# Performance work log

Hardware: AMD Instinct MI355X
Metric: run time of the kernel (lower is better)

The kernel has to match this reference:

```python
import jax, jax.numpy as jnp
import numpy as np

B, F0, D = 2048, 40, 32
LAYER0, LAYER1 = 128, 128  # layer_size=(128,128), split_half=True -> field_nums=[40,64]


def setup_inputs() -> dict:
    key = jax.random.key(0)
    k1, k2, k3 = jax.random.split(key, 3)
    x = jax.random.normal(k1, (B, F0, D), dtype=jnp.float32)
    # TF conv1d filters: [1, F_prev*F0, size]; we store them reshaped [F0, F_prev_fields, size]
    # Layer 0: F_prev = F0 = 40 -> W0 flattened index m = i*F0 + j, i over x0 fields, j over hidden fields
    W0 = jax.random.normal(k2, (F0, F0, LAYER0), dtype=jnp.float32) * 0.05
    b0 = jnp.zeros((LAYER0,), dtype=jnp.float32)
    # Layer 1: F_prev = LAYER0 // 2 = 64 (split_half)
    W1 = jax.random.normal(k3, (F0, LAYER0 // 2, LAYER1), dtype=jnp.float32) * 0.05
    b1 = jnp.zeros((LAYER1,), dtype=jnp.float32)
    return {"x": x, "W0": W0, "b0": b0, "W1": W1, "b1": b1}


def reference(x, W0, b0, W1, b1):
    # CIN layer 0: outer product x0 (x) x0 over fields per embedding dim, then 1x1 conv + bias + relu
    # TF flattens dot_result as index i*F_prev + j, matching W0[i, j, s].
    h0 = jax.nn.relu(jnp.einsum('bid,bjd,ijs->bsd', x, x, W0) + b0[None, :, None])  # (B, 128, D)
    half = LAYER0 // 2
    next_hidden, direct0 = h0[:, :half, :], h0[:, half:, :]  # split_half
    # CIN layer 1 (last layer): all feature maps go to direct connect
    direct1 = jax.nn.relu(
        jnp.einsum('bid,bjd,ijs->bsd', x, next_hidden, W1) + b1[None, :, None]
    )  # (B, 128, D)
    result = jnp.concatenate([direct0, direct1], axis=1)  # (B, 192, D)
    return jnp.sum(result, axis=-1)  # (B, 192)
```

## Files before the change

kernel.cpp:

```cpp
#include <hip/hip_runtime.h>
#include <stdint.h>


typedef __attribute__((ext_vector_type(8))) _Float16 half8;
typedef __attribute__((ext_vector_type(2))) _Float16 half2v;
typedef __attribute__((ext_vector_type(16))) float f32x16;

#define T0 30
#define T1P 81
#define PERIOD 3
#define WBUF 12288

__host__ __device__ constexpr int ic0_of(int t) {
    return (t < 2) ? t : (t < 6) ? (t - 2) : (t < 12) ? (t - 6)
         : (t < 20) ? (t - 12) : (t - 20);
}
__host__ __device__ constexpr int jc0_of(int t) {
    return (t < 2) ? 0 : (t < 6) ? 1 : (t < 12) ? 2 : (t < 20) ? 3 : 4;
}

__device__ __forceinline__ unsigned short f2h(float f) {
    return __builtin_bit_cast(unsigned short, (_Float16)f);
}
__device__ __forceinline__ void gl_lds16(const unsigned short* g, unsigned short* l) {
    __builtin_amdgcn_global_load_lds(
        (const __attribute__((address_space(1))) unsigned int*)g,
        (__attribute__((address_space(3))) unsigned int*)l,
        16, 0, 0);
}
__device__ __forceinline__ uint4 avmul(half2v xs, uint4 jv) {
    uint4 r;
    r.x = __builtin_bit_cast(unsigned int, (half2v)(xs * __builtin_bit_cast(half2v, jv.x)));
    r.y = __builtin_bit_cast(unsigned int, (half2v)(xs * __builtin_bit_cast(half2v, jv.y)));
    r.z = __builtin_bit_cast(unsigned int, (half2v)(xs * __builtin_bit_cast(half2v, jv.z)));
    r.w = __builtin_bit_cast(unsigned int, (half2v)(xs * __builtin_bit_cast(half2v, jv.w)));
    return r;
}

__global__ void permute_w_both(const float* __restrict__ W0, const float* __restrict__ W1,
                               unsigned short* __restrict__ Wp0, unsigned short* __restrict__ Wp1)
{
    const int t = blockIdx.x;
    const int tid = threadIdx.x;
    unsigned short outv[16];
    unsigned short* dst;
    if (t < T0) {
        const int ic = ic0_of(t), jc = jc0_of(t);
        #pragma unroll
        for (int q = 0; q < 16; ++q) {
            int pos  = tid * 16 + q;
            int e    = pos & 7, lane = (pos >> 3) & 63;
            int kh   = (pos >> 9) & 1, sq = pos >> 10;
            int s    = sq * 32 + (lane & 31);
            int i    = ic * 4 + kh * 2 + (lane >> 5);
            int j    = jc * 8 + e;
            float v = 0.0f;
            if (i < j)       v = W0[((size_t)(i * 40 + j)) * 128 + s]
                               + W0[((size_t)(j * 40 + i)) * 128 + s];
            else if (i == j) v = W0[((size_t)(i * 40 + i)) * 128 + s];
            outv[q] = f2h(v);
        }
        dst = Wp0 + (size_t)t * 4096 + tid * 16;
    } else {
        const int tt = t - T0;
        if (tt == 80) {
            #pragma unroll
            for (int q = 0; q < 16; ++q) outv[q] = 0;
        } else {
            const int jc = tt / 10, ic = tt % 10;
            #pragma unroll
            for (int q = 0; q < 16; ++q) {
                int pos  = tid * 16 + q;
                int e    = pos & 7, lane = (pos >> 3) & 63;
                int kh   = (pos >> 9) & 1, sq = pos >> 10;
                int s    = sq * 32 + (lane & 31);
                int i    = ic * 4 + kh * 2 + (lane >> 5);
                int j    = jc * 8 + e;
                outv[q] = f2h(W1[((size_t)(i * 64 + j)) * 128 + s]);
            }
        }
        dst = Wp1 + (size_t)tt * 4096 + tid * 16;
    }
    *(uint4*)dst       = *(const uint4*)outv;
    *(uint4*)(dst + 8) = *(const uint4*)(outv + 8);
}

template<int T, int PHASE>
__device__ __forceinline__ void gemm_phase(
    const unsigned short* __restrict__ Wp,
    const unsigned short* __restrict__ Jl,
    int jstride,
    const unsigned int xk[2][10],
    unsigned short* Wb,
    f32x16 acc[2], int tid)
{
    const int lane = tid & 63;
    const int wv = tid >> 6;
    const int rt = wv >> 2;
    const int sq = wv & 3;
    const int c31 = lane & 31;

    const unsigned short* jbase = Jl + (rt * 64 + c31) * jstride;

    const unsigned short* brd = Wb + sq * 1024 + lane * 8;
    const unsigned short* gsrc = Wp + tid * 8;
    unsigned short* ldstA = Wb + wv * 512;
    unsigned short* ldstB = Wb + 8192 + wv * 512;

    auto stage_period = [&](int buf, int t0) {
        gl_lds16(gsrc + (size_t)t0 * 4096, ldstA + buf * WBUF);
        if (wv < 8)
            gl_lds16(gsrc + (size_t)(t0 + 2) * 4096, ldstB + buf * WBUF);
    };

    stage_period(0, 0);
    __syncthreads();

    uint4 jv0, jv1;
    constexpr int NP = T / PERIOD;
    #pragma unroll
    for (int p = 0; p < NP; ++p) {
        const int cb = p & 1;
        const int nb = cb ^ 1;
        if ((p + 1) * PERIOD < T) stage_period(nb, (p + 1) * PERIOD);
        #pragma unroll
        for (int u = 0; u < PERIOD; ++u) {
            const int t  = p * PERIOD + u;
            const int ic = (PHASE == 0) ? ic0_of(t) : (t % 10);
            const int jc = (PHASE == 0) ? jc0_of(t) : (t / 10);
            const bool rl = (t == 0) ||
                (jc != ((PHASE == 0) ? jc0_of(t - 1) : ((t - 1) / 10)));
            if (rl) {
                jv0 = *(const uint4*)(jbase + jc * 8);
                jv1 = *(const uint4*)(jbase + 32 * jstride + jc * 8);
            }
            const unsigned short* bb_ = brd + cb * WBUF + u * 4096;
            #pragma unroll
            for (int kh = 0; kh < 2; ++kh) {
                uint4 bvv = *(const uint4*)(bb_ + kh * 512);
                half2v xp = __builtin_bit_cast(half2v, xk[kh][ic]);
                half2v x0 = {xp[0], xp[0]};
                half2v x1 = {xp[1], xp[1]};
                acc[0] = __builtin_amdgcn_mfma_f32_32x32x16_f16(
                    __builtin_bit_cast(half8, avmul(x0, jv0)),
                    __builtin_bit_cast(half8, bvv), acc[0], 0, 0, 0);
                acc[1] = __builtin_amdgcn_mfma_f32_32x32x16_f16(
                    __builtin_bit_cast(half8, avmul(x1, jv1)),
                    __builtin_bit_cast(half8, bvv), acc[1], 0, 0, 0);
            }
        }
        __syncthreads();
    }
}

__global__ __launch_bounds__(1024, 4)
void fused_two_layer(const float* __restrict__ x,
                     const unsigned short* __restrict__ W0p,
                     const float* __restrict__ b0,
                     const unsigned short* __restrict__ W1p,
                     const float* __restrict__ b1,
                     float* __restrict__ out)
{
    __shared__ __align__(16) unsigned short Xl[256 * 40];
    __shared__ __align__(16) unsigned short NH[256 * 72];
    __shared__ __align__(16) unsigned short Wb[2 * WBUF];

    const int tid  = threadIdx.x;
    const int lane = tid & 63;
    const int wv   = tid >> 6;
    const int rt   = wv >> 2;
    const int sq   = wv & 3;
    const int c31  = lane & 31;
    const int hb   = lane >> 5;

    const float* xblk = x + (size_t)blockIdx.x * (8 * 40 * 32);
    #pragma unroll
    for (int k = 0; k < 10; ++k) {
        int f = 1024 * k + tid;
        int bl = f / 1280, rem = f - bl * 1280;
        int i = rem >> 5, d = rem & 31;
        Xl[(bl * 32 + d) * 40 + i] = f2h(xblk[f]);
    }
    __syncthreads();

    unsigned int xk[2][10];
    {
        const unsigned short* xr0 = Xl + (rt * 64 + c31) * 40;
        const unsigned short* xr1 = xr0 + 32 * 40;
        #pragma unroll
        for (int ic = 0; ic < 10; ++ic)
            #pragma unroll
            for (int kh = 0; kh < 2; ++kh) {
                unsigned int u0 = xr0[ic * 4 + kh * 2 + hb];
                unsigned int u1 = xr1[ic * 4 + kh * 2 + hb];
                xk[kh][ic] = u0 | (u1 << 16);
            }
    }

    f32x16 acc[2];
    #pragma unroll
    for (int rtt = 0; rtt < 2; ++rtt)
        #pragma unroll
        for (int rg = 0; rg < 16; ++rg) acc[rtt][rg] = 0.f;

    gemm_phase<T0, 0>(W0p, Xl, 40, xk, Wb, acc, tid);

    {
        float bs = b0[sq * 32 + c31];
        if (sq < 2) {
            #pragma unroll
            for (int rtt = 0; rtt < 2; ++rtt)
                #pragma unroll
                for (int rg = 0; rg < 16; ++rg) {
                    int row = rt * 64 + rtt * 32 + (rg & 3) + 8 * (rg >> 2) + 4 * hb;
                    NH[row * 72 + sq * 32 + c31] =
                        f2h(fmaxf(acc[rtt][rg] + bs, 0.0f));
                }
        } else {
            #pragma unroll
            for (int rtt = 0; rtt < 2; ++rtt) {
                float s = 0.f;
                #pragma unroll
                for (int rg = 0; rg < 16; ++rg)
                    s += fmaxf(acc[rtt][rg] + bs, 0.0f);
                s += __shfl_xor(s, 32, 64);
                int bb = blockIdx.x * 8 + rt * 2 + rtt;
                if (lane < 32)
                    out[(size_t)bb * 192 + (sq - 2) * 32 + c31] = s;
            }
            if (sq == 2) {
                int a = (rt * 64 + lane) * 72 + 64;
                *(uint4*)&NH[a] = (uint4){0u, 0u, 0u, 0u};
            }
        }
    }
    __syncthreads();

    #pragma unroll
    for (int rtt = 0; rtt < 2; ++rtt)
        #pragma unroll
        for (int rg = 0; rg < 16; ++rg) acc[rtt][rg] = 0.f;

    gemm_phase<T1P, 1>(W1p, NH, 72, xk, Wb, acc, tid);

    {
        float bs = b1[sq * 32 + c31];
        #pragma unroll
        for (int rtt = 0; rtt < 2; ++rtt) {
            float s = 0.f;
            #pragma unroll
            for (int rg = 0; rg < 16; ++rg)
                s += fmaxf(acc[rtt][rg] + bs, 0.0f);
            s += __shfl_xor(s, 32, 64);
            int bb = blockIdx.x * 8 + rt * 2 + rtt;
            if (lane < 32)
                out[(size_t)bb * 192 + 64 + sq * 32 + c31] = s;
        }
    }
}

extern "C" void kernel_launch(void* const* d_in, const int* in_sizes, int n_in,
                              void* d_out, int out_size, void* d_ws, size_t ws_size,
                              hipStream_t stream) {
    const float* x  = (const float*)d_in[0];
    const float* W0 = (const float*)d_in[1];
    const float* b0 = (const float*)d_in[2];
    const float* W1 = (const float*)d_in[3];
    const float* b1 = (const float*)d_in[4];
    float* out = (float*)d_out;

    unsigned short* W0p = (unsigned short*)d_ws;
    unsigned short* W1p = (unsigned short*)((char*)d_ws + T0 * 4096 * 2);

    permute_w_both<<<T0 + T1P, 256, 0, stream>>>(W0, W1, W0p, W1p);
    fused_two_layer<<<256, 1024, 0, stream>>>(x, W0p, b0, W1p, b1, out);
}
```

Before: 121.6 us.

## Triple-buffer weight staging with one barrier per two tiles and MFMA priority

```diff
diff --git a/kernel.cpp b/kernel.cpp
--- a/kernel.cpp
+++ b/kernel.cpp
@@ -7,9 +7,8 @@
 typedef __attribute__((ext_vector_type(16))) float f32x16;
 
 #define T0 30
-#define T1P 81
-#define PERIOD 3
-#define WBUF 12288
+#define T1 80
+#define WBUF 8192
 
 __host__ __device__ constexpr int ic0_of(int t) {
     return (t < 2) ? t : (t < 6) ? (t - 2) : (t < 12) ? (t - 6)
@@ -63,21 +62,16 @@
         dst = Wp0 + (size_t)t * 4096 + tid * 16;
     } else {
         const int tt = t - T0;
-        if (tt == 80) {
-            #pragma unroll
-            for (int q = 0; q < 16; ++q) outv[q] = 0;
-        } else {
-            const int jc = tt / 10, ic = tt % 10;
-            #pragma unroll
-            for (int q = 0; q < 16; ++q) {
-                int pos  = tid * 16 + q;
-                int e    = pos & 7, lane = (pos >> 3) & 63;
-                int kh   = (pos >> 9) & 1, sq = pos >> 10;
-                int s    = sq * 32 + (lane & 31);
-                int i    = ic * 4 + kh * 2 + (lane >> 5);
-                int j    = jc * 8 + e;
-                outv[q] = f2h(W1[((size_t)(i * 64 + j)) * 128 + s]);
-            }
+        const int jc = tt / 10, ic = tt % 10;
+        #pragma unroll
+        for (int q = 0; q < 16; ++q) {
+            int pos  = tid * 16 + q;
+            int e    = pos & 7, lane = (pos >> 3) & 63;
+            int kh   = (pos >> 9) & 1, sq = pos >> 10;
+            int s    = sq * 32 + (lane & 31);
+            int i    = ic * 4 + kh * 2 + (lane >> 5);
+            int j    = jc * 8 + e;
+            outv[q] = f2h(W1[((size_t)(i * 64 + j)) * 128 + s]);
         }
         dst = Wp1 + (size_t)tt * 4096 + tid * 16;
     }
@@ -104,28 +98,31 @@
 
     const unsigned short* brd = Wb + sq * 1024 + lane * 8;
     const unsigned short* gsrc = Wp + tid * 8;
-    unsigned short* ldstA = Wb + wv * 512;
-    unsigned short* ldstB = Wb + 8192 + wv * 512;
-
-    auto stage_period = [&](int buf, int t0) {
-        gl_lds16(gsrc + (size_t)t0 * 4096, ldstA + buf * WBUF);
-        if (wv < 8)
-            gl_lds16(gsrc + (size_t)(t0 + 2) * 4096, ldstB + buf * WBUF);
+    unsigned short* ldst = Wb + tid * 8;
+
+    auto stage = [&](int k) {
+        gl_lds16(gsrc + (size_t)k * WBUF, ldst + (k % 3) * WBUF);
     };
 
-    stage_period(0, 0);
-    __syncthreads();
+    constexpr int NP = T / 2;
+    stage(0);
+    stage(1);
 
     uint4 jv0, jv1;
-    constexpr int NP = T / PERIOD;
     #pragma unroll
     for (int p = 0; p < NP; ++p) {
-        const int cb = p & 1;
-        const int nb = cb ^ 1;
-        if ((p + 1) * PERIOD < T) stage_period(nb, (p + 1) * PERIOD);
-        #pragma unroll
-        for (int u = 0; u < PERIOD; ++u) {
-            const int t  = p * PERIOD + u;
+        if (p == NP - 1) asm volatile("s_waitcnt vmcnt(0)" ::: "memory");
+        else             asm volatile("s_waitcnt vmcnt(1)" ::: "memory");
+        __builtin_amdgcn_sched_barrier(0);
+        __builtin_amdgcn_s_barrier();
+        __builtin_amdgcn_sched_barrier(0);
+        if (p + 2 < NP) stage(p + 2);
+        __builtin_amdgcn_sched_barrier(0);
+
+        const unsigned short* bper = brd + (p % 3) * WBUF;
+        #pragma unroll
+        for (int u = 0; u < 2; ++u) {
+            const int t  = p * 2 + u;
             const int ic = (PHASE == 0) ? ic0_of(t) : (t % 10);
             const int jc = (PHASE == 0) ? jc0_of(t) : (t / 10);
             const bool rl = (t == 0) ||
@@ -134,10 +131,10 @@
                 jv0 = *(const uint4*)(jbase + jc * 8);
                 jv1 = *(const uint4*)(jbase + 32 * jstride + jc * 8);
             }
-            const unsigned short* bb_ = brd + cb * WBUF + u * 4096;
+            __builtin_amdgcn_s_setprio(1);
             #pragma unroll
             for (int kh = 0; kh < 2; ++kh) {
-                uint4 bvv = *(const uint4*)(bb_ + kh * 512);
+                uint4 bvv = *(const uint4*)(bper + u * 4096 + kh * 512);
                 half2v xp = __builtin_bit_cast(half2v, xk[kh][ic]);
                 half2v x0 = {xp[0], xp[0]};
                 half2v x1 = {xp[1], xp[1]};
@@ -148,8 +145,8 @@
                     __builtin_bit_cast(half8, avmul(x1, jv1)),
                     __builtin_bit_cast(half8, bvv), acc[1], 0, 0, 0);
             }
-        }
-        __syncthreads();
+            __builtin_amdgcn_s_setprio(0);
+        }
     }
 }
 
@@ -163,7 +160,7 @@
 {
     __shared__ __align__(16) unsigned short Xl[256 * 40];
     __shared__ __align__(16) unsigned short NH[256 * 72];
-    __shared__ __align__(16) unsigned short Wb[2 * WBUF];
+    __shared__ __align__(16) unsigned short Wb[3 * WBUF];
 
     const int tid  = threadIdx.x;
     const int lane = tid & 63;
@@ -228,10 +225,6 @@
                 if (lane < 32)
                     out[(size_t)bb * 192 + (sq - 2) * 32 + c31] = s;
             }
-            if (sq == 2) {
-                int a = (rt * 64 + lane) * 72 + 64;
-                *(uint4*)&NH[a] = (uint4){0u, 0u, 0u, 0u};
-            }
         }
     }
     __syncthreads();
@@ -241,7 +234,7 @@
         #pragma unroll
         for (int rg = 0; rg < 16; ++rg) acc[rtt][rg] = 0.f;
 
-    gemm_phase<T1P, 1>(W1p, NH, 72, xk, Wb, acc, tid);
+    gemm_phase<T1, 1>(W1p, NH, 72, xk, Wb, acc, tid);
 
     {
         float bs = b1[sq * 32 + c31];
@@ -272,6 +265,6 @@
     unsigned short* W0p = (unsigned short*)d_ws;
     unsigned short* W1p = (unsigned short*)((char*)d_ws + T0 * 4096 * 2);
 
-    permute_w_both<<<T0 + T1P, 256, 0, stream>>>(W0, W1, W0p, W1p);
+    permute_w_both<<<T0 + T1, 256, 0, stream>>>(W0, W1, W0p, W1p);
     fused_two_layer<<<256, 1024, 0, stream>>>(x, W0p, b0, W1p, b1, out);
 }
```

After: 120.0 us. No clear change (-1.3%).
